# Performance work log

Measured on AMD Instinct MI355X. Metric: run time of the kernel, lower is better.

## Reference

```python
import jax, jax.numpy as jnp
import numpy as np

B, L, C = 2, 8192, 1536
P, W, H, F = 512, 16, 32, 128
POS = 32  # pos_channels (even, half=16 <= P-1)
EPS = 1e-5


def central_mask_features(seq_len, feat):
    # static numpy construction (matches torch central_mask_features)
    half = feat // 2
    rel = np.arange(2 * seq_len - 1, dtype=np.float64) - (seq_len - 1)
    widths = np.arange(half, dtype=np.float64) + np.geomspace(1, seq_len - half + 1, half, endpoint=False)
    onehot = (widths[None, :] > np.abs(rel)[:, None]).astype(np.float32)
    sign = np.sign(rel)[:, None].astype(np.float32)
    return jnp.asarray(np.concatenate([onehot, onehot * sign], axis=-1))  # [2P-1, POS]


def relative_shift(x):
    # x: [B, H, S, 2S-1] -> [B, H, S, S]
    b, h, s, d = x.shape
    x = jnp.pad(x, ((0, 0), (0, 0), (0, 0), (1, 0)))
    x = x.reshape(b, h, d + 1, s)[:, :, 1:, :].reshape(b, h, s, d)
    return x[..., :s]


def setup_inputs() -> dict:
    key = jax.random.key(0)
    ks = jax.random.split(key, 12)
    s = 0.02
    return {
        "x": jax.random.normal(ks[0], (B, L, C), jnp.float32),
        "norm_scale": jnp.ones((C,), jnp.float32),
        "norm_ms": jnp.ones((C,), jnp.float32),
        "Wq": jax.random.normal(ks[1], (C, H * F), jnp.float32) * s,
        "Wk": jax.random.normal(ks[2], (C, H * F), jnp.float32) * s,
        "Wp": jax.random.normal(ks[3], (POS, H * F), jnp.float32) * s,
        "bp": jax.random.normal(ks[4], (H * F,), jnp.float32) * s,
        "q_r_bias": jnp.zeros((1, 1, H, F), jnp.float32),
        "k_r_bias": jnp.zeros((1, 1, H, F), jnp.float32),
        "Wyq": jax.random.normal(ks[5], (C, F), jnp.float32) * s,
        "Wyk": jax.random.normal(ks[6], (C, F), jnp.float32) * s,
        "Wout": jax.random.normal(ks[7], (H, F), jnp.float32) * s,
        "bout": jax.random.normal(ks[8], (F,), jnp.float32) * s,
    }


def reference(x, norm_scale, norm_ms, Wq, Wk, Wp, bp, q_r_bias, k_r_bias, Wyq, Wyk, Wout, bout):
    b = x.shape[0]
    # AvgPool1d(kernel=stride=W) along sequence: [B,L,C] -> [B,P,C]
    xp = x.reshape(b, P, W, C).mean(axis=2)
    # EMA RMS batch norm (inference): per-channel rsqrt of running mean-square, learned scale
    xn = xp * (norm_scale * jax.lax.rsqrt(norm_ms + EPS))
    q = (xn @ Wq).reshape(b, P, H, F)
    k = (xn @ Wk).reshape(b, P, H, F)
    pos_feat = central_mask_features(P, POS)                     # [2P-1, POS]
    pos_enc = (pos_feat @ Wp + bp).reshape(2 * P - 1, H, F)      # [2P-1, H, F]
    rel_q = jnp.einsum('bqhc,phc->bhqp', q + q_r_bias, pos_enc) / 2
    rel_q = relative_shift(rel_q).transpose(0, 2, 3, 1)          # [B,Q,K,H]
    rel_k = jnp.einsum('bkhc,phc->bhkp', k + k_r_bias, pos_enc) / 2
    rel_k = relative_shift(rel_k).transpose(0, 2, 3, 1)          # [B,K,Q,H]
    a = jnp.einsum('bqhc,bkhc->bqkh', q, k) + 0.5 * (rel_q + rel_k.transpose(0, 2, 1, 3))
    xa = jax.nn.gelu(xn, approximate=False)
    y_q = xa @ Wyq                                               # [B,P,F]
    y_k = xa @ Wyk
    pair = jnp.einsum('bqkh,hf->bqkf', a, Wout) + bout + y_q[:, :, None, :] + y_k[:, None, :, :]
    return pair  # dropout p=0 / eval -> identity
```

## Files before the change

### kernel.cpp

```cpp
#include <hip/hip_runtime.h>
#include <math.h>

typedef unsigned short u16;
typedef __attribute__((ext_vector_type(8))) short short8;
typedef __attribute__((ext_vector_type(4))) float f32x4;

#define BB 2
#define LL 8192
#define CC 1536
#define PP 512
#define WW 16
#define HH 32
#define FF 128
#define HF 4096
#define NBANDS 33

__device__ __forceinline__ float bf2f(u16 u){
  union { unsigned int i; float f; } v; v.i = ((unsigned int)u) << 16; return v.f;
}
__device__ __forceinline__ u16 f2bf(float f){
  union { float f; unsigned int i; } v; v.f = f;
  unsigned int x = v.i;
  return (u16)((x + 0x7fffu + ((x >> 16) & 1u)) >> 16);
}
__device__ __forceinline__ float ld_in(const void* p, size_t i, int is32){
  return is32 ? ((const float*)p)[i] : bf2f(((const u16*)p)[i]);
}
__device__ __forceinline__ int probe32(const void* ms){
  return ((const unsigned int*)ms)[0] == 0x3F800000u ? 1 : 0;
}

__global__ void k_bands(int* jt){
  int a = threadIdx.x;
  if (a < 512){
    double lw = log(497.0) / 16.0;
    int j = 0;
    for (int i = 0; i < 16; ++i){
      double w = (double)i + exp(lw * (double)i);
      if (w <= (double)a) j++;
    }
    jt[a] = j;
  }
}

__global__ void k_pool(const void* __restrict__ x, const void* __restrict__ ns,
                       const void* __restrict__ ms, u16* __restrict__ xn,
                       u16* __restrict__ xa){
  const int is32 = probe32(ms);
  int row = blockIdx.x;
  int b = row >> 9, p = row & 511;
  size_t base = ((size_t)(b*LL + p*WW)) * CC;
  for (int c = threadIdx.x; c < CC; c += 256){
    float s = 0.f;
    for (int w = 0; w < WW; ++w) s += ld_in(x, base + (size_t)w*CC + c, is32);
    float xp = s * (1.f/16.f);
    float sc = ld_in(ns, c, is32) * rsqrtf(ld_in(ms, c, is32) + 1e-5f);
    float v = xp * sc;
    xn[(size_t)row*CC + c] = f2bf(v);
    float g = 0.5f * v * (1.f + erff(v * 0.70710678118654752f));
    xa[(size_t)row*CC + c] = f2bf(g);
  }
}

__global__ void k_transpose(const void* __restrict__ in, u16* __restrict__ out,
                            int R, int Ccols, const void* __restrict__ msp){
  const int is32 = probe32(msp);
  __shared__ u16 tbuf[32][33];
  int c0 = blockIdx.x * 32, r0 = blockIdx.y * 32;
  int tx = threadIdx.x & 31, ty = threadIdx.x >> 5;
  for (int p = 0; p < 4; ++p)
    tbuf[ty + p*8][tx] = f2bf(ld_in(in, (size_t)(r0 + ty + p*8)*Ccols + c0 + tx, is32));
  __syncthreads();
  for (int p = 0; p < 4; ++p)
    out[(size_t)(c0 + ty + p*8)*R + r0 + tx] = tbuf[tx][ty + p*8];
}

__launch_bounds__(256)
__global__ void k_gemm(const u16* __restrict__ A, const u16* __restrict__ BT0,
                       const u16* __restrict__ BT1, u16* __restrict__ C0,
                       u16* __restrict__ C1){
  const u16* BT = blockIdx.z ? BT1 : BT0;
  u16* Cc = blockIdx.z ? C1 : C0;
  __shared__ u16 As[128*40];
  __shared__ u16 Bs[128*40];
  const int n0 = blockIdx.x * 128, m0 = blockIdx.y * 128;
  const int t = threadIdx.x, lane = t & 63, wave = t >> 6;
  const int lm = lane & 15, lq = lane >> 4;
  const int srow = t >> 1, scol = (t & 1) << 4;
  f32x4 acc[2][8];
  for (int a = 0; a < 2; ++a)
    for (int b = 0; b < 8; ++b) acc[a][b] = (f32x4){0.f,0.f,0.f,0.f};
  for (int k0 = 0; k0 < CC; k0 += 32){
    short8 va0 = *(const short8*)&A [(size_t)(m0+srow)*CC + k0 + scol];
    short8 va1 = *(const short8*)&A [(size_t)(m0+srow)*CC + k0 + scol + 8];
    short8 vb0 = *(const short8*)&BT[(size_t)(n0+srow)*CC + k0 + scol];
    short8 vb1 = *(const short8*)&BT[(size_t)(n0+srow)*CC + k0 + scol + 8];
    *(short8*)&As[srow*40 + scol]     = va0;
    *(short8*)&As[srow*40 + scol + 8] = va1;
    *(short8*)&Bs[srow*40 + scol]     = vb0;
    *(short8*)&Bs[srow*40 + scol + 8] = vb1;
    __syncthreads();
    short8 af[2], bfr[8];
    af[0] = *(const short8*)&As[(wave*32 + lm)*40 + lq*8];
    af[1] = *(const short8*)&As[(wave*32 + 16 + lm)*40 + lq*8];
    for (int nt = 0; nt < 8; ++nt)
      bfr[nt] = *(const short8*)&Bs[(nt*16 + lm)*40 + lq*8];
    for (int mt = 0; mt < 2; ++mt)
      for (int nt = 0; nt < 8; ++nt)
        acc[mt][nt] = __builtin_amdgcn_mfma_f32_16x16x32_bf16(af[mt], bfr[nt], acc[mt][nt], 0, 0, 0);
    __syncthreads();
  }
  for (int mt = 0; mt < 2; ++mt)
    for (int nt = 0; nt < 8; ++nt)
      for (int r = 0; r < 4; ++r){
        int gr = m0 + wave*32 + mt*16 + lq*4 + r;
        int gc = n0 + nt*16 + lm;
        Cc[(size_t)gr*HF + gc] = f2bf(acc[mt][nt][r]);
      }
}

__launch_bounds__(256)
__global__ void k_ygemm(const u16* __restrict__ A, const u16* __restrict__ BT,
                        float* __restrict__ yq, float* __restrict__ yk){
  __shared__ u16 As[128*40];
  __shared__ u16 Bs[128*40];
  const int n0 = blockIdx.x * 128, m0 = blockIdx.y * 128;
  const int t = threadIdx.x, lane = t & 63, wave = t >> 6;
  const int lm = lane & 15, lq = lane >> 4;
  const int srow = t >> 1, scol = (t & 1) << 4;
  f32x4 acc[2][8];
  for (int a = 0; a < 2; ++a)
    for (int b = 0; b < 8; ++b) acc[a][b] = (f32x4){0.f,0.f,0.f,0.f};
  for (int k0 = 0; k0 < CC; k0 += 32){
    short8 va0 = *(const short8*)&A [(size_t)(m0+srow)*CC + k0 + scol];
    short8 va1 = *(const short8*)&A [(size_t)(m0+srow)*CC + k0 + scol + 8];
    short8 vb0 = *(const short8*)&BT[(size_t)(n0+srow)*CC + k0 + scol];
    short8 vb1 = *(const short8*)&BT[(size_t)(n0+srow)*CC + k0 + scol + 8];
    *(short8*)&As[srow*40 + scol]     = va0;
    *(short8*)&As[srow*40 + scol + 8] = va1;
    *(short8*)&Bs[srow*40 + scol]     = vb0;
    *(short8*)&Bs[srow*40 + scol + 8] = vb1;
    __syncthreads();
    short8 af[2], bfr[8];
    af[0] = *(const short8*)&As[(wave*32 + lm)*40 + lq*8];
    af[1] = *(const short8*)&As[(wave*32 + 16 + lm)*40 + lq*8];
    for (int nt = 0; nt < 8; ++nt)
      bfr[nt] = *(const short8*)&Bs[(nt*16 + lm)*40 + lq*8];
    for (int mt = 0; mt < 2; ++mt)
      for (int nt = 0; nt < 8; ++nt)
        acc[mt][nt] = __builtin_amdgcn_mfma_f32_16x16x32_bf16(af[mt], bfr[nt], acc[mt][nt], 0, 0, 0);
    __syncthreads();
  }
  for (int mt = 0; mt < 2; ++mt)
    for (int nt = 0; nt < 8; ++nt)
      for (int r = 0; r < 4; ++r){
        int gr = m0 + wave*32 + mt*16 + lq*4 + r;
        int gc = n0 + nt*16 + lm;
        if (gc < FF) yq[(size_t)gr*FF + gc] = acc[mt][nt][r];
        else         yk[(size_t)gr*FF + gc - FF] = acc[mt][nt][r];
      }
}

__launch_bounds__(256)
__global__ void k_rel(const u16* __restrict__ qk, const void* __restrict__ rbias,
                      const void* __restrict__ Wp, const void* __restrict__ bp,
                      float* __restrict__ Dg, const void* __restrict__ msp){
  const int is32 = probe32(msp);
  __shared__ u16 As[128*136];
  __shared__ u16 Bs[48*136];
  const int r0 = blockIdx.x * 128;
  const int h  = blockIdx.y;
  const int t = threadIdx.x, lane = t & 63, wave = t >> 6;
  const int lm = lane & 15, lq = lane >> 4;

  for (int v = 0; v < 8; ++v){
    int idx = (t + v*256) * 8;
    int r = idx >> 7, c = idx & 127;
    short8 s8 = *(const short8*)&qk[(size_t)(r0 + r)*HF + h*FF + c];
    short8 o;
    for (int j = 0; j < 8; ++j)
      o[j] = (short)f2bf(bf2f((u16)s8[j]) + ld_in(rbias, (size_t)h*FF + c + j, is32));
    *(short8*)&As[r*136 + c] = o;
  }
  for (int idx = t; idx < 48*128; idx += 256){
    int i = idx >> 7, c = idx & 127;
    float v;
    if (i < 32)       v = ld_in(Wp, (size_t)i*HF + h*FF + c, is32);
    else if (i == 32) v = ld_in(bp, (size_t)h*FF + c, is32);
    else              v = 0.f;
    Bs[i*136 + c] = f2bf(v);
  }
  __syncthreads();

  f32x4 acc[2][3];
  for (int mt = 0; mt < 2; ++mt)
    for (int nt = 0; nt < 3; ++nt) acc[mt][nt] = (f32x4){0.f,0.f,0.f,0.f};
  for (int ks = 0; ks < 4; ++ks){
    short8 af[2], bfr[3];
    for (int mt = 0; mt < 2; ++mt)
      af[mt] = *(const short8*)&As[(wave*32 + mt*16 + lm)*136 + ks*32 + lq*8];
    for (int nt = 0; nt < 3; ++nt)
      bfr[nt] = *(const short8*)&Bs[(nt*16 + lm)*136 + ks*32 + lq*8];
    for (int mt = 0; mt < 2; ++mt)
      for (int nt = 0; nt < 3; ++nt)
        acc[mt][nt] = __builtin_amdgcn_mfma_f32_16x16x32_bf16(af[mt], bfr[nt], acc[mt][nt], 0, 0, 0);
  }
  for (int mt = 0; mt < 2; ++mt)
    for (int nt = 0; nt < 3; ++nt)
      for (int rr = 0; rr < 4; ++rr){
        int row = r0 + wave*32 + mt*16 + lq*4 + rr;
        int i = nt*16 + lm;
        if (i < 33)
          Dg[((size_t)row*32 + h)*33 + i] = acc[mt][nt][rr];
      }
}

__launch_bounds__(256)
__global__ void k_coef(const float* __restrict__ Dg, const float* __restrict__ yrow,
                       const void* __restrict__ Wo, const void* __restrict__ bout,
                       u16* __restrict__ Cout, const void* __restrict__ msp){
  const int is32 = probe32(msp);
  __shared__ float A1[4*32*17];
  __shared__ float A2[4*32*17];
  __shared__ float A0[4*32];
  __shared__ u16 coef[144*40];
  const int row0 = blockIdx.x * 4;
  const int t = threadIdx.x;

  {
    int r = t >> 6, h = (t >> 1) & 31, sel = t & 1;
    size_t dbase = ((size_t)(row0 + r)*32 + h)*33 + sel*16;
    float d[16];
    for (int j = 0; j < 16; ++j) d[j] = Dg[dbase + j];
    float* Aout = sel ? A2 : A1;
    int base = (r*32 + h)*17;
    float run = 0.f;
    for (int j = 16; j >= 0; --j){
      Aout[base + j] = run;
      if (j > 0) run += d[j-1];
    }
    if (!sel) A0[r*32 + h] = Dg[dbase + 32];
  }
  __syncthreads();
  for (int m = t; m < 144*32; m += 256){
    int h = m & 31; int row = m >> 5;
    if (row >= 132){ coef[row*40 + h] = 0; continue; }
    int r = row / 33; int band = row - r*33;
    float a0 = A0[r*32 + h];
    int base = (r*32 + h)*17;
    float val;
    if (band == 0)       val = A1[base] + a0;
    else if (band <= 16) val = A1[base + band] + A2[base + band] + a0;
    else                 val = A1[base + band - 16] - A2[base + band - 16] + a0;
    coef[row*40 + h] = f2bf(0.25f * val);
  }
  __syncthreads();
  const int lane = t & 63, wave = t >> 6, lm = lane & 15, lq = lane >> 4;
  short8 wf[8];
  float bo[8];
  for (int ft = 0; ft < 8; ++ft){
    short8 v;
    for (int j = 0; j < 8; ++j)
      v[j] = (short)f2bf(ld_in(Wo, (size_t)(lq*8 + j)*FF + ft*16 + lm, is32));
    wf[ft] = v;
    bo[ft] = 0.5f * ld_in(bout, ft*16 + lm, is32);
  }
  for (int mt = wave; mt < 9; mt += 4){
    short8 af = *(const short8*)&coef[(mt*16 + lm)*40 + lq*8];
    f32x4 d[8];
    for (int ft = 0; ft < 8; ++ft)
      d[ft] = __builtin_amdgcn_mfma_f32_16x16x32_bf16(af, wf[ft], (f32x4){0.f,0.f,0.f,0.f}, 0, 0, 0);
    for (int rr = 0; rr < 4; ++rr){
      int row = mt*16 + lq*4 + rr;
      if (row < 132){
        int r = row / 33; int band = row - r*33;
        const float* yr = yrow + (size_t)(row0 + r)*FF;
        u16* co = Cout + ((size_t)(row0 + r)*NBANDS + band)*FF;
        for (int ft = 0; ft < 8; ++ft){
          int f = ft*16 + lm;
          co[f] = f2bf(d[ft][rr] + yr[f] + bo[ft]);
        }
      }
    }
  }
}

__launch_bounds__(512, 4)
__global__ void k_pair(const u16* __restrict__ qb, const u16* __restrict__ kbm,
                       const u16* __restrict__ Cq, const u16* __restrict__ Ck,
                       const void* __restrict__ Wo, const int* __restrict__ jt,
                       float* __restrict__ out, const void* __restrict__ msp){
  const int is32 = probe32(msp);
  __shared__ u16 atile[1024*32];
  __shared__ int jt_lds[512];
  const int bz = blockIdx.z;
  const int q0 = blockIdx.y * 32, k0 = blockIdx.x * 32;
  const int t = threadIdx.x, lane = t & 63, wave = t >> 6;
  const int lm = lane & 15, lq = lane >> 4;
  const u16* qbase = qb  + (size_t)(bz*PP + q0)*HF;
  const u16* kbase = kbm + (size_t)(bz*PP + k0)*HF;
  if (t < 512) jt_lds[t] = jt[t];
  for (int hh = 0; hh < 4; ++hh){
    int h = wave*4 + hh;
    short8 af[2][4], bfr[2][4];
    for (int qm = 0; qm < 2; ++qm)
      for (int ks = 0; ks < 4; ++ks)
        af[qm][ks] = *(const short8*)&qbase[(size_t)(qm*16 + lm)*HF + h*FF + ks*32 + lq*8];
    for (int kn = 0; kn < 2; ++kn)
      for (int ks = 0; ks < 4; ++ks)
        bfr[kn][ks] = *(const short8*)&kbase[(size_t)(kn*16 + lm)*HF + h*FF + ks*32 + lq*8];
    int hg = h >> 3, hl = h & 7;
    for (int qm = 0; qm < 2; ++qm)
      for (int kn = 0; kn < 2; ++kn){
        f32x4 acc = (f32x4){0.f,0.f,0.f,0.f};
        for (int ks = 0; ks < 4; ++ks)
          acc = __builtin_amdgcn_mfma_f32_16x16x32_bf16(af[qm][ks], bfr[kn][ks], acc, 0, 0, 0);
        for (int r = 0; r < 4; ++r){
          int pair = (qm*16 + lq*4 + r)*32 + kn*16 + lm;
          atile[pair*32 + ((hg ^ (pair & 3)) << 3) + hl] = f2bf(acc[r]);
        }
      }
  }
  short8 wf[8];
  for (int ft = 0; ft < 8; ++ft){
    short8 v;
    for (int j = 0; j < 8; ++j)
      v[j] = (short)f2bf(ld_in(Wo, (size_t)(lq*8 + j)*FF + ft*16 + lm, is32));
    wf[ft] = v;
  }
  __syncthreads();
  short8 afr[8];
  for (int rr = 0; rr < 8; ++rr){
    int pr = (wave*8 + rr)*16 + lm;
    afr[rr] = *(const short8*)&atile[pr*32 + ((lq ^ (pr & 3)) << 3)];
  }
  float* dsl = (float*)&atile[wave*128*32];
  const int dQK = k0 - q0;
  for (int rr = 0; rr < 8; ++rr){
    int rg = wave*8 + rr;
    for (int ft = 0; ft < 8; ++ft){
      f32x4 d = __builtin_amdgcn_mfma_f32_16x16x32_bf16(afr[rr], wf[ft], (f32x4){0.f,0.f,0.f,0.f}, 0, 0, 0);
      for (int r = 0; r < 4; ++r)
        dsl[(lq*4 + r)*128 + ft*16 + lm] = d[r];
    }
    asm volatile("s_waitcnt lgkmcnt(0)" ::: "memory");
    for (int p2 = 0; p2 < 4; ++p2){
      int plocal = p2*4 + lq;
      int pair_g = rg*16 + plocal;
      int qi = pair_g >> 5, ki = pair_g & 31;
      int dd = dQK + ki - qi;
      int ad = dd < 0 ? -dd : dd;
      int j = jt_lds[ad];
      int cqb, ckb;
      if (dd == 0){ cqb = 0; ckb = 0; }
      else if (dd > 0){ cqb = j; ckb = 16 + j; }
      else { cqb = 16 + j; ckb = j; }
      int Q = q0 + qi, Kg = k0 + ki;
      int f0 = lm * 8;
      const u16* cqrow = Cq + ((size_t)((bz*PP + Q)*NBANDS + cqb))*FF + f0;
      const u16* ckrow = Ck + ((size_t)((bz*PP + Kg)*NBANDS + ckb))*FF + f0;
      float* orow = out + ((size_t)(bz*PP + Q)*PP + Kg)*FF + f0;
      short8 cqv = *(const short8*)cqrow;
      short8 ckv = *(const short8*)ckrow;
      f32x4 d0 = *(const f32x4*)&dsl[plocal*128 + f0];
      f32x4 d1 = *(const f32x4*)&dsl[plocal*128 + f0 + 4];
      f32x4 o0, o1;
      for (int u = 0; u < 4; ++u){
        o0[u] = d0[u] + bf2f((u16)cqv[u])     + bf2f((u16)ckv[u]);
        o1[u] = d1[u] + bf2f((u16)cqv[u + 4]) + bf2f((u16)ckv[u + 4]);
      }
      *(f32x4*)&orow[0] = o0;
      *(f32x4*)&orow[4] = o1;
    }
  }
}

extern "C" void kernel_launch(void* const* d_in, const int* in_sizes, int n_in,
                              void* d_out, int out_size, void* d_ws, size_t ws_size,
                              hipStream_t stream){
  const void* x   = d_in[0];
  const void* ns  = d_in[1];
  const void* ms  = d_in[2];
  const void* Wq  = d_in[3];
  const void* Wk  = d_in[4];
  const void* Wp  = d_in[5];
  const void* bp  = d_in[6];
  const void* qrb = d_in[7];
  const void* krb = d_in[8];
  const void* Wyq = d_in[9];
  const void* Wyk = d_in[10];
  const void* Wo  = d_in[11];
  const void* bo  = d_in[12];
  float* out = (float*)d_out;

  char* ws = (char*)d_ws;
  size_t off = 0;
  auto take = [&](size_t bytes) -> char* {
    char* p = ws + off;
    off += (bytes + 255) & ~(size_t)255;
    return p;
  };
  u16*  xn   = (u16*)take((size_t)1024*CC*2);
  u16*  xa   = (u16*)take((size_t)1024*CC*2);
  u16*  qbuf = (u16*)take((size_t)1024*HF*2);
  u16*  kbuf = (u16*)take((size_t)1024*HF*2);
  u16*  WqT  = (u16*)take((size_t)HF*CC*2);
  u16*  WkT  = (u16*)take((size_t)HF*CC*2);
  u16*  WyT  = (u16*)take((size_t)2*FF*CC*2);
  float* yq  = (float*)take((size_t)1024*FF*4);
  float* yk  = (float*)take((size_t)1024*FF*4);
  u16*  Cqb  = (u16*)take((size_t)1024*NBANDS*FF*2);
  u16*  Ckb  = (u16*)take((size_t)1024*NBANDS*FF*2);
  int*  jt   = (int*)take((size_t)512*4);
  float* Dq = (float*)WqT;
  float* Dk = (float*)WkT;

  hipLaunchKernelGGL(k_bands, dim3(1), dim3(512), 0, stream, jt);
  hipLaunchKernelGGL(k_pool, dim3(1024), dim3(256), 0, stream, x, ns, ms, xn, xa);
  hipLaunchKernelGGL(k_transpose, dim3(128, 48), dim3(256), 0, stream, Wq, WqT, CC, HF, ms);
  hipLaunchKernelGGL(k_transpose, dim3(128, 48), dim3(256), 0, stream, Wk, WkT, CC, HF, ms);
  hipLaunchKernelGGL(k_transpose, dim3(4, 48), dim3(256), 0, stream, Wyq, WyT, CC, FF, ms);
  hipLaunchKernelGGL(k_transpose, dim3(4, 48), dim3(256), 0, stream, Wyk, WyT + (size_t)FF*CC, CC, FF, ms);
  hipLaunchKernelGGL(k_gemm, dim3(32, 8, 2), dim3(256), 0, stream, xn, WqT, WkT, qbuf, kbuf);
  hipLaunchKernelGGL(k_ygemm, dim3(2, 8), dim3(256), 0, stream, xa, WyT, yq, yk);
  hipLaunchKernelGGL(k_rel, dim3(8, 32), dim3(256), 0, stream, qbuf, qrb, Wp, bp, Dq, ms);
  hipLaunchKernelGGL(k_rel, dim3(8, 32), dim3(256), 0, stream, kbuf, krb, Wp, bp, Dk, ms);
  hipLaunchKernelGGL(k_coef, dim3(256), dim3(256), 0, stream, Dq, yq, Wo, bo, Cqb, ms);
  hipLaunchKernelGGL(k_coef, dim3(256), dim3(256), 0, stream, Dk, yk, Wo, bo, Ckb, ms);
  hipLaunchKernelGGL(k_pair, dim3(16, 16, 2), dim3(512), 0, stream, qbuf, kbuf, Cqb, Ckb, Wo, jt, out, ms);
}
```

Before: 784.5 us.

## Transpose pair-projection MFMA to skip LDS staging and vectorize pooling loads

The second MFMA in k_pair now swaps its operands (Wout fragment as A, attention tile as B), so each lane holds output features for a single pair. The epilogue can then add the bias bands and write straight from registers, which removes the LDS round trip through the dsl buffer and its waitcnt. The per-head stores into the attention tile are packed two heads per 32-bit write under a new XOR swizzle key to cut LDS write instructions and bank conflicts. The pooling kernel is also vectorized to four channels per thread. The output stores become 16-byte chunks strided by 64 bytes within a row, which may coalesce less well than the earlier contiguous 32-byte-per-lane stores.

Measured after the change: 711.0 us. -9.4%, faster.

```diff
diff --git a/kernel.cpp b/kernel.cpp
--- a/kernel.cpp
+++ b/kernel.cpp
@@ -2,8 +2,10 @@
 #include <math.h>
 
 typedef unsigned short u16;
+typedef unsigned int u32;
 typedef __attribute__((ext_vector_type(8))) short short8;
 typedef __attribute__((ext_vector_type(4))) float f32x4;
+typedef __attribute__((ext_vector_type(4))) unsigned short us4;
 
 #define BB 2
 #define LL 8192
@@ -50,15 +52,31 @@
   int row = blockIdx.x;
   int b = row >> 9, p = row & 511;
   size_t base = ((size_t)(b*LL + p*WW)) * CC;
-  for (int c = threadIdx.x; c < CC; c += 256){
-    float s = 0.f;
-    for (int w = 0; w < WW; ++w) s += ld_in(x, base + (size_t)w*CC + c, is32);
-    float xp = s * (1.f/16.f);
-    float sc = ld_in(ns, c, is32) * rsqrtf(ld_in(ms, c, is32) + 1e-5f);
-    float v = xp * sc;
-    xn[(size_t)row*CC + c] = f2bf(v);
-    float g = 0.5f * v * (1.f + erff(v * 0.70710678118654752f));
-    xa[(size_t)row*CC + c] = f2bf(g);
+  for (int c4 = threadIdx.x; c4 < CC/4; c4 += 256){
+    int c = c4 * 4;
+    f32x4 s = (f32x4){0.f,0.f,0.f,0.f};
+    if (is32){
+      const float* xp = (const float*)x + base + c;
+      for (int w = 0; w < WW; ++w)
+        s += *(const f32x4*)(xp + (size_t)w*CC);
+    } else {
+      const u16* xp = (const u16*)x + base + c;
+      for (int w = 0; w < WW; ++w){
+        us4 v = *(const us4*)(xp + (size_t)w*CC);
+        for (int u = 0; u < 4; ++u) s[u] += bf2f(v[u]);
+      }
+    }
+    us4 on, oa;
+    for (int u = 0; u < 4; ++u){
+      float xp4 = s[u] * (1.f/16.f);
+      float sc = ld_in(ns, c+u, is32) * rsqrtf(ld_in(ms, c+u, is32) + 1e-5f);
+      float v = xp4 * sc;
+      on[u] = f2bf(v);
+      float g = 0.5f * v * (1.f + erff(v * 0.70710678118654752f));
+      oa[u] = f2bf(g);
+    }
+    *(us4*)&xn[(size_t)row*CC + c] = on;
+    *(us4*)&xa[(size_t)row*CC + c] = oa;
   }
 }
 
@@ -299,27 +317,37 @@
   const int lm = lane & 15, lq = lane >> 4;
   const u16* qbase = qb  + (size_t)(bz*PP + q0)*HF;
   const u16* kbase = kbm + (size_t)(bz*PP + k0)*HF;
-  if (t < 512) jt_lds[t] = jt[t];
-  for (int hh = 0; hh < 4; ++hh){
-    int h = wave*4 + hh;
-    short8 af[2][4], bfr[2][4];
+  u32* atile32 = (u32*)atile;
+  jt_lds[t & 511] = jt[t & 511];
+  for (int hp = 0; hp < 2; ++hp){
+    f32x4 acc2[2][2][2];
+    for (int e = 0; e < 2; ++e){
+      int h = wave*4 + hp*2 + e;
+      short8 af[2][4], bfr[2][4];
+      for (int qm = 0; qm < 2; ++qm)
+        for (int ks = 0; ks < 4; ++ks)
+          af[qm][ks] = *(const short8*)&qbase[(size_t)(qm*16 + lm)*HF + h*FF + ks*32 + lq*8];
+      for (int kn = 0; kn < 2; ++kn)
+        for (int ks = 0; ks < 4; ++ks)
+          bfr[kn][ks] = *(const short8*)&kbase[(size_t)(kn*16 + lm)*HF + h*FF + ks*32 + lq*8];
+      for (int qm = 0; qm < 2; ++qm)
+        for (int kn = 0; kn < 2; ++kn){
+          f32x4 acc = (f32x4){0.f,0.f,0.f,0.f};
+          for (int ks = 0; ks < 4; ++ks)
+            acc = __builtin_amdgcn_mfma_f32_16x16x32_bf16(af[qm][ks], bfr[kn][ks], acc, 0, 0, 0);
+          acc2[e][qm][kn] = acc;
+        }
+    }
+    int h0 = wave*4 + hp*2;
+    int hg = h0 >> 3, hl0 = h0 & 7;
     for (int qm = 0; qm < 2; ++qm)
-      for (int ks = 0; ks < 4; ++ks)
-        af[qm][ks] = *(const short8*)&qbase[(size_t)(qm*16 + lm)*HF + h*FF + ks*32 + lq*8];
-    for (int kn = 0; kn < 2; ++kn)
-      for (int ks = 0; ks < 4; ++ks)
-        bfr[kn][ks] = *(const short8*)&kbase[(size_t)(kn*16 + lm)*HF + h*FF + ks*32 + lq*8];
-    int hg = h >> 3, hl = h & 7;
-    for (int qm = 0; qm < 2; ++qm)
-      for (int kn = 0; kn < 2; ++kn){
-        f32x4 acc = (f32x4){0.f,0.f,0.f,0.f};
-        for (int ks = 0; ks < 4; ++ks)
-          acc = __builtin_amdgcn_mfma_f32_16x16x32_bf16(af[qm][ks], bfr[kn][ks], acc, 0, 0, 0);
+      for (int kn = 0; kn < 2; ++kn)
         for (int r = 0; r < 4; ++r){
           int pair = (qm*16 + lq*4 + r)*32 + kn*16 + lm;
-          atile[pair*32 + ((hg ^ (pair & 3)) << 3) + hl] = f2bf(acc[r]);
+          int key = (pair & 3) ^ ((pair >> 7) & 3);
+          u32 pk = (u32)f2bf(acc2[0][qm][kn][r]) | ((u32)f2bf(acc2[1][qm][kn][r]) << 16);
+          atile32[pair*16 + ((hg ^ key) << 2) + (hl0 >> 1)] = pk;
         }
-      }
   }
   short8 wf[8];
   for (int ft = 0; ft < 8; ++ft){
@@ -329,48 +357,40 @@
     wf[ft] = v;
   }
   __syncthreads();
-  short8 afr[8];
-  for (int rr = 0; rr < 8; ++rr){
-    int pr = (wave*8 + rr)*16 + lm;
-    afr[rr] = *(const short8*)&atile[pr*32 + ((lq ^ (pr & 3)) << 3)];
-  }
-  float* dsl = (float*)&atile[wave*128*32];
   const int dQK = k0 - q0;
   for (int rr = 0; rr < 8; ++rr){
     int rg = wave*8 + rr;
+    int pr = rg*16 + lm;
+    int key = (pr & 3) ^ ((pr >> 7) & 3);
+    short8 afr = *(const short8*)&atile[pr*32 + ((lq ^ key) << 3)];
+    int qi = pr >> 5, ki = pr & 31;
+    int dd = dQK + ki - qi;
+    int ad = dd < 0 ? -dd : dd;
+    int j = jt_lds[ad];
+    int cqb, ckb;
+    if (dd == 0){ cqb = 0; ckb = 0; }
+    else if (dd > 0){ cqb = j; ckb = 16 + j; }
+    else { cqb = 16 + j; ckb = j; }
+    int Q = q0 + qi, Kg = k0 + ki;
+    const u16* cqrow = Cq + ((size_t)((bz*PP + Q)*NBANDS + cqb))*FF + lq*4;
+    const u16* ckrow = Ck + ((size_t)((bz*PP + Kg)*NBANDS + ckb))*FF + lq*4;
+    float* orow = out + ((size_t)(bz*PP + Q)*PP + Kg)*FF + lq*4;
+    us4 cqv[8], ckv[8];
     for (int ft = 0; ft < 8; ++ft){
-      f32x4 d = __builtin_amdgcn_mfma_f32_16x16x32_bf16(afr[rr], wf[ft], (f32x4){0.f,0.f,0.f,0.f}, 0, 0, 0);
-      for (int r = 0; r < 4; ++r)
-        dsl[(lq*4 + r)*128 + ft*16 + lm] = d[r];
-    }
-    asm volatile("s_waitcnt lgkmcnt(0)" ::: "memory");
-    for (int p2 = 0; p2 < 4; ++p2){
-      int plocal = p2*4 + lq;
-      int pair_g = rg*16 + plocal;
-      int qi = pair_g >> 5, ki = pair_g & 31;
-      int dd = dQK + ki - qi;
-      int ad = dd < 0 ? -dd : dd;
-      int j = jt_lds[ad];
-      int cqb, ckb;
-      if (dd == 0){ cqb = 0; ckb = 0; }
-      else if (dd > 0){ cqb = j; ckb = 16 + j; }
-      else { cqb = 16 + j; ckb = j; }
-      int Q = q0 + qi, Kg = k0 + ki;
-      int f0 = lm * 8;
-      const u16* cqrow = Cq + ((size_t)((bz*PP + Q)*NBANDS + cqb))*FF + f0;
-      const u16* ckrow = Ck + ((size_t)((bz*PP + Kg)*NBANDS + ckb))*FF + f0;
-      float* orow = out + ((size_t)(bz*PP + Q)*PP + Kg)*FF + f0;
-      short8 cqv = *(const short8*)cqrow;
-      short8 ckv = *(const short8*)ckrow;
-      f32x4 d0 = *(const f32x4*)&dsl[plocal*128 + f0];
-      f32x4 d1 = *(const f32x4*)&dsl[plocal*128 + f0 + 4];
-      f32x4 o0, o1;
-      for (int u = 0; u < 4; ++u){
-        o0[u] = d0[u] + bf2f((u16)cqv[u])     + bf2f((u16)ckv[u]);
-        o1[u] = d1[u] + bf2f((u16)cqv[u + 4]) + bf2f((u16)ckv[u + 4]);
-      }
-      *(f32x4*)&orow[0] = o0;
-      *(f32x4*)&orow[4] = o1;
+      cqv[ft] = *(const us4*)&cqrow[ft*16];
+      ckv[ft] = *(const us4*)&ckrow[ft*16];
+    }
+    for (int g = 0; g < 2; ++g){
+      f32x4 dts[4];
+      for (int f4 = 0; f4 < 4; ++f4)
+        dts[f4] = __builtin_amdgcn_mfma_f32_16x16x32_bf16(wf[g*4 + f4], afr, (f32x4){0.f,0.f,0.f,0.f}, 0, 0, 0);
+      for (int f4 = 0; f4 < 4; ++f4){
+        int ft = g*4 + f4;
+        f32x4 o;
+        for (int u = 0; u < 4; ++u)
+          o[u] = dts[f4][u] + bf2f(cqv[ft][u]) + bf2f(ckv[ft][u]);
+        *(f32x4*)&orow[ft*16] = o;
+      }
     }
   }
 }
```
